# Optimization experiments

Measured on AMD Instinct MI355X. Metric: run time of the kernel, lower is better.

Reference implementation:

```python
import jax, jax.numpy as jnp
import numpy as np

NINP, NHID, NOUT, DT = 128, 768, 128, 1.0
T, B = 256, 256


def setup_inputs() -> dict:
    key = jax.random.key(0)
    ks = jax.random.split(key, 9)
    std = 1.0 / np.sqrt(NHID)
    u = lambda k, shape: jax.random.uniform(k, shape, jnp.float32, -std, std)
    return {
        "input": jax.random.normal(ks[0], (T, B, NINP), jnp.float32),
        "W_inp": u(ks[1], (4 * NHID, NINP)),
        "b_inp": u(ks[2], (4 * NHID,)),
        "W_hid": u(ks[3], (3 * NHID, NHID)),
        "b_hid": u(ks[4], (3 * NHID,)),
        "W_z": u(ks[5], (NHID, NHID)),
        "b_z": u(ks[6], (NHID,)),
        "W_cls": jax.random.normal(ks[7], (NOUT, NHID), jnp.float32) * np.sqrt(2.0 / NHID),
        "b_cls": u(ks[8], (NOUT,)),
    }


def reference(input, W_inp, b_inp, W_hid, b_hid, W_z, b_z, W_cls, b_cls):
    # Precompute input projections for all timesteps: [T, B, 4*NHID]
    inp_proj = jnp.einsum('tbi,hi->tbh', input, W_inp) + b_inp

    def step(carry, xi):
        y, z = carry
        hid = y @ W_hid.T + b_hid                     # [B, 3*NHID]
        i_dt1, i_dt2, i_z, i_y = jnp.split(xi, 4, axis=1)
        h_dt1, h_dt2, h_y = jnp.split(hid, 3, axis=1)
        ms_dt_bar = DT * jax.nn.sigmoid(i_dt1 + h_dt1)
        ms_dt = DT * jax.nn.sigmoid(i_dt2 + h_dt2)
        z = (1.0 - ms_dt) * z + ms_dt * jnp.tanh(i_y + h_y)
        y = (1.0 - ms_dt_bar) * y + ms_dt_bar * jnp.tanh(z @ W_z.T + b_z + i_z)
        return (y, z), None

    y0 = jnp.zeros((input.shape[1], NHID), input.dtype)
    z0 = jnp.zeros_like(y0)
    (y, z), _ = jax.lax.scan(step, (y0, z0), inp_proj)
    return y @ W_cls.T + b_cls
```

## Files before the change

### kernel.cpp

```cpp
#include <hip/hip_runtime.h>
#include <stdint.h>


#define NINP 128
#define NHID 768
#define NOUT 128
#define T_STEPS 256
#define BATCH 256

#define NGRP 8
#define CBLK 24
#define NBLK 192
#define NTHR 256

#define NHTILES 144
#define SBUF 196608
#define WZ_ELEMS (1152 * 512)
#define WI_ELEMS (768 * 512)

typedef short bf16x8 __attribute__((ext_vector_type(8)));
typedef float f32x4 __attribute__((ext_vector_type(4)));

__device__ __forceinline__ unsigned short f2b(float f) {
  union { float f; unsigned u; } x; x.f = f;
  return (unsigned short)((x.u + 0x7fffu + ((x.u >> 16) & 1u)) >> 16);
}
__device__ __forceinline__ float b2f(unsigned short h) {
  union { unsigned u; float f; } x; x.u = ((unsigned)h) << 16; return x.f;
}
__device__ __forceinline__ float fsig(float x) { return 1.0f / (1.0f + __expf(-x)); }
__device__ __forceinline__ float ftanh(float x) {
  float e = __expf(2.0f * x);
  return 1.0f - 2.0f / (e + 1.0f);
}

#define MFMA16(a, b, c) __builtin_amdgcn_mfma_f32_16x16x32_bf16(a, b, c, 0, 0, 0)

#define AL32(p) __hip_atomic_load((const unsigned*)(p), __ATOMIC_RELAXED, __HIP_MEMORY_SCOPE_AGENT)
#define AS32(p, v) __hip_atomic_store((unsigned*)(p), (v), __ATOMIC_RELAXED, __HIP_MEMORY_SCOPE_AGENT)

__device__ __forceinline__ void uld16(bf16x8* dst, const unsigned short* addr) {
  asm volatile("global_load_dwordx4 %0, %1, off sc0 sc1" : "=v"(*dst) : "v"(addr));
}
__device__ __forceinline__ void cld16(bf16x8* dst, const unsigned short* addr) {
  asm volatile("global_load_dwordx4 %0, %1, off" : "=v"(*dst) : "v"(addr));
}
__device__ __forceinline__ void ust16(unsigned short* addr, bf16x8 v) {
  asm volatile("global_store_dwordx4 %0, %1, off sc0 sc1" :: "v"(addr), "v"(v) : "memory");
}
#define WAITV(N) do { \
  asm volatile("s_waitcnt vmcnt(" #N ")" ::: "memory"); \
  __builtin_amdgcn_sched_barrier(0); } while (0)

__device__ __forceinline__ void split8(const float* p, bf16x8* hi, bf16x8* lo) {
  union { bf16x8 v; unsigned short s[8]; } H, L;
#pragma unroll
  for (int e = 0; e < 8; ++e) {
    float v = p[e];
    unsigned short h = f2b(v);
    H.s[e] = h;
    L.s[e] = f2b(v - b2f(h));
  }
  *hi = H.v; *lo = L.v;
}

__global__ __launch_bounds__(256) void conv_w(
    const float* __restrict__ W_z, const float* __restrict__ W_inp,
    unsigned short* __restrict__ Wz, unsigned short* __restrict__ Wi) {
  int idx = blockIdx.x * 256 + threadIdx.x;
  int t = idx >> 9, r = idx & 511;
  int ll = r >> 3, e = r & 7;
  int col16 = ll & 15;
  int kk = ((ll >> 4) * 8) + e;
  if (t < 1152) {
    int kt = t % 24, ct = (t / 24) & 1, c = t / 48;
    Wz[idx] = f2b(W_z[(size_t)(c * 32 + ct * 16 + col16) * NHID + kt * 32 + kk]);
  } else {
    int u = t - 1152;
    int xkt = u & 3, ct = (u >> 2) & 1, seg = (u >> 3) & 3, c = u >> 5;
    Wi[(size_t)u * 512 + r] =
        f2b(W_inp[(size_t)(seg * NHID + c * 32 + ct * 16 + col16) * NINP + xkt * 32 + kk]);
  }
}

__global__ __launch_bounds__(256) void xprep(
    const float* __restrict__ x, unsigned short* __restrict__ XF) {
  int gid = blockIdx.x * 256 + threadIdx.x;
  int lane = gid & 63;
  int rtx = (gid >> 6) & 15;
  int xkt = (gid >> 10) & 3;
  int t = gid >> 12;
  int kg = lane >> 4, r16 = lane & 15;
  int row = rtx * 16 + r16;
  bf16x8 hi, lo;
  split8(x + ((size_t)t * BATCH + row) * NINP + xkt * 32 + kg * 8, &hi, &lo);
  size_t lo_off = (size_t)kg * 128 + r16 * 8;
  *(bf16x8*)(XF + ((((size_t)t * 2 + 0) * 4 + xkt) * 16 + rtx) * 512 + lo_off) = hi;
  *(bf16x8*)(XF + ((((size_t)t * 2 + 1) * 4 + xkt) * 16 + rtx) * 512 + lo_off) = lo;
}

__global__ __launch_bounds__(NTHR, 1) void lem_kernel(
    const float* __restrict__ b_inp,
    const float* __restrict__ W_hid,
    const float* __restrict__ b_hid,
    const float* __restrict__ b_z,
    const float* __restrict__ W_cls,
    const float* __restrict__ b_cls,
    float* __restrict__ out,
    unsigned short* __restrict__ Y,
    unsigned short* __restrict__ Z,
    unsigned* __restrict__ flags,
    const unsigned short* __restrict__ Wz,
    const unsigned short* __restrict__ Wi,
    const unsigned short* __restrict__ XF)
{
  __shared__ unsigned short wlds[NHTILES * 512];
  __shared__ float red[128 * 24];
  __shared__ unsigned short zt[2 * 512];

  const int tid = threadIdx.x;
  const int l   = tid & 63;
  const int w   = tid >> 6;
  const int rtl = w & 1;
  const int kh  = w >> 1;
  const int g   = blockIdx.x / CBLK;
  const int c   = blockIdx.x % CBLK;
  const int colbase = c * 32;
  const int lc  = l & 15;
  const int kg8 = (l >> 4) * 8;
  const int laneoff = (l >> 4) * 128 + lc * 8;
  const int rtg = g * 2 + rtl;
  const int r16b = (l >> 4) * 4;

  for (int idx = tid; idx < NHTILES * 512; idx += NTHR) {
    int t = idx >> 9;
    int r = idx & 511;
    int ll = r >> 3, e = r & 7;
    int col16 = ll & 15;
    int kk = ((ll >> 4) * 8) + e;
    int kt = t % 24, cs = t / 24;
    int ct = cs / 3, seg = cs % 3;
    wlds[idx] = f2b(W_hid[(size_t)(seg * NHID + colbase + ct * 16 + col16) * NHID + kt * 32 + kk]);
  }

#define LDSB(t) (*(const bf16x8*)&wlds[((t) << 9) + (l << 3)])

  float c1[2], c2[2], cy[2], cz[2];
#pragma unroll
  for (int ct = 0; ct < 2; ++ct) {
    int col = colbase + ct * 16 + lc;
    c1[ct] = b_inp[col] + b_hid[col];
    c2[ct] = b_inp[NHID + col] + b_hid[NHID + col];
    cy[ct] = b_inp[3 * NHID + col] + b_hid[2 * NHID + col];
    cz[ct] = b_inp[2 * NHID + col] + b_z[col];
  }
  unsigned* gfA = flags + g * 128;
  unsigned* gfB = gfA + 64;
  const int khb = kh * 12;
  unsigned short* Zc = Z + (size_t)(c * 16 + rtg) * 512;
  unsigned short* Yc = Y + (size_t)(c * 16 + rtg) * 512;

  bf16x8 wifA[3][2][2];
  bf16x8 wiB[2][2];
#pragma unroll
  for (int hseg = 0; hseg < 3; ++hseg) {
    int wseg = (hseg == 2) ? 3 : hseg;
#pragma unroll
    for (int ct = 0; ct < 2; ++ct)
#pragma unroll
      for (int xk2 = 0; xk2 < 2; ++xk2)
        cld16(&wifA[hseg][ct][xk2],
              Wi + (size_t)((((c * 4 + wseg) * 2 + ct) * 4) + (kh * 2 + xk2)) * 512 + l * 8);
  }
#pragma unroll
  for (int ct = 0; ct < 2; ++ct)
#pragma unroll
    for (int xk2 = 0; xk2 < 2; ++xk2)
      cld16(&wiB[ct][xk2],
            Wi + (size_t)((((c * 4 + 2) * 2 + ct) * 4) + (kh * 2 + xk2)) * 512 + l * 8);

  bf16x8 xa[4];
#define ISSUE_XA(sidx) do { \
    cld16(&xa[0], XF + ((((size_t)(sidx) * 2 + 0) * 4 + (kh * 2 + 0)) * 16 + rtg) * 512 + laneoff); \
    cld16(&xa[1], XF + ((((size_t)(sidx) * 2 + 1) * 4 + (kh * 2 + 0)) * 16 + rtg) * 512 + laneoff); \
    cld16(&xa[2], XF + ((((size_t)(sidx) * 2 + 0) * 4 + (kh * 2 + 1)) * 16 + rtg) * 512 + laneoff); \
    cld16(&xa[3], XF + ((((size_t)(sidx) * 2 + 1) * 4 + (kh * 2 + 1)) * 16 + rtg) * 512 + laneoff); } while (0)

  ISSUE_XA(0);
  WAITV(0);
  __syncthreads();

  f32x4 yloc[2], zloc[2], msb[2];
#pragma unroll
  for (int ct = 0; ct < 2; ++ct) { yloc[ct] = f32x4{0,0,0,0}; zloc[ct] = f32x4{0,0,0,0}; }

  float* rp = red + (rtl * 64 + l) * 24;
  unsigned short* trow = zt + rtl * 512;

  bf16x8 ybufs[6][2];
  bf16x8 zbuf[6];
  bf16x8 wzf[6][2];
  const unsigned short* wzb0 = Wz + (size_t)((c * 2 + 0) * 24) * 512 + l * 8;
  const unsigned short* wzb1 = Wz + (size_t)((c * 2 + 1) * 24) * 512 + l * 8;

#define ISSUE_Y(slot, j) do { \
    int kt_ = khb + 2 * (j); \
    uld16(&ybufs[slot][0], Y + (size_t)(kt_ * 16 + rtg) * 512 + laneoff); \
    uld16(&ybufs[slot][1], Y + (size_t)((kt_ + 1) * 16 + rtg) * 512 + laneoff); } while (0)

#define ISSUE_Z(slot, j) do { \
    int kt_ = khb + (j); \
    uld16(&zbuf[slot], Z + (size_t)(kt_ * 16 + rtg) * 512 + laneoff); \
    cld16(&wzf[slot][0], wzb0 + (size_t)kt_ * 512); \
    cld16(&wzf[slot][1], wzb1 + (size_t)kt_ * 512); } while (0)

  for (int s = 0; s < T_STEPS; ++s) {
    f32x4 h[3][2];
#pragma unroll
    for (int sg = 0; sg < 3; ++sg)
#pragma unroll
      for (int ct = 0; ct < 2; ++ct) h[sg][ct] = f32x4{0,0,0,0};

    ISSUE_Y(0, 0); ISSUE_Y(1, 1); ISSUE_Y(2, 2);
    ISSUE_Y(3, 3); ISSUE_Y(4, 4); ISSUE_Y(5, 5);
    WAITV(12);
#pragma unroll
    for (int xk2 = 0; xk2 < 2; ++xk2)
#pragma unroll
      for (int sg = 0; sg < 3; ++sg)
#pragma unroll
        for (int ct = 0; ct < 2; ++ct) {
          h[sg][ct] = MFMA16(xa[xk2 * 2 + 0], wifA[sg][ct][xk2], h[sg][ct]);
          h[sg][ct] = MFMA16(xa[xk2 * 2 + 1], wifA[sg][ct][xk2], h[sg][ct]);
        }
#pragma unroll
    for (int j = 0; j < 6; ++j) {
      if (j == 0) { WAITV(10); } else if (j == 1) { WAITV(8); }
      else if (j == 2) { WAITV(6); } else if (j == 3) { WAITV(4); }
      else if (j == 4) { WAITV(2); } else { WAITV(0); }
#pragma unroll
      for (int i2 = 0; i2 < 2; ++i2) {
        int ktp = khb + 2 * j + i2;
        bf16x8 a = ybufs[j][i2];
#pragma unroll
        for (int ct = 0; ct < 2; ++ct)
#pragma unroll
          for (int sg = 0; sg < 3; ++sg)
            h[sg][ct] = MFMA16(a, LDSB((ct * 3 + sg) * 24 + ktp), h[sg][ct]);
      }
    }
    if (kh == 1) {
#pragma unroll
      for (int sg = 0; sg < 3; ++sg)
#pragma unroll
        for (int ct = 0; ct < 2; ++ct)
          *(f32x4*)(rp + (sg * 2 + ct) * 4) = h[sg][ct];
    }
    __syncthreads();
    if (kh == 0) {
#pragma unroll
      for (int sg = 0; sg < 3; ++sg)
#pragma unroll
        for (int ct = 0; ct < 2; ++ct)
          h[sg][ct] += *(const f32x4*)(rp + (sg * 2 + ct) * 4);
#pragma unroll
      for (int ct = 0; ct < 2; ++ct)
#pragma unroll
        for (int i = 0; i < 4; ++i) {
          float a1 = fsig(h[0][ct][i] + c1[ct]);
          float a2 = fsig(h[1][ct][i] + c2[ct]);
          float gg = ftanh(h[2][ct][i] + cy[ct]);
          float zn = (1.0f - a2) * zloc[ct][i] + a2 * gg;
          zloc[ct][i] = zn;
          msb[ct][i] = a1;
          int jj = ct * 16 + lc;
          trow[((jj >> 3) * 16 + r16b + i) * 8 + (jj & 7)] = f2b(zn);
        }
      asm volatile("s_waitcnt lgkmcnt(0)" ::: "memory");
      __builtin_amdgcn_sched_barrier(0);
      bf16x8 zrun = *(const bf16x8*)(trow + l * 8);
      ust16(Zc + l * 8, zrun);
    }
    __syncthreads();
    if (tid == 0) AS32(&gfA[c], (unsigned)(s + 1));
    if (w == 0) {
      const unsigned* fp = gfA + (l < CBLK ? l : 0);
      while (true) {
        unsigned v = AL32(fp);
        if (__all((l >= CBLK) || (v >= (unsigned)(s + 1)))) break;
        __builtin_amdgcn_s_sleep(1);
      }
    }
    __syncthreads();

    f32x4 az[2];
    az[0] = f32x4{0,0,0,0}; az[1] = f32x4{0,0,0,0};
    ISSUE_Z(0, 0); ISSUE_Z(1, 1); ISSUE_Z(2, 2); ISSUE_Z(3, 3); ISSUE_Z(4, 4);
#pragma unroll
    for (int xk2 = 0; xk2 < 2; ++xk2)
#pragma unroll
      for (int ct = 0; ct < 2; ++ct) {
        az[ct] = MFMA16(xa[xk2 * 2 + 0], wiB[ct][xk2], az[ct]);
        az[ct] = MFMA16(xa[xk2 * 2 + 1], wiB[ct][xk2], az[ct]);
      }
#pragma unroll
    for (int j = 0; j < 12; ++j) {
      if (j < 7) ISSUE_Z((j + 5) % 6, j + 5);
      if (j < 7) { WAITV(15); } else if (j == 7) { WAITV(12); }
      else if (j == 8) { WAITV(9); } else if (j == 9) { WAITV(6); }
      else if (j == 10) { WAITV(3); } else { WAITV(0); }
      const int sl = j % 6;
      az[0] = MFMA16(zbuf[sl], wzf[sl][0], az[0]);
      az[1] = MFMA16(zbuf[sl], wzf[sl][1], az[1]);
    }
    if (kh == 1) {
      *(f32x4*)(rp + 0) = az[0];
      *(f32x4*)(rp + 4) = az[1];
    }
    __syncthreads();
    if (kh == 0) {
      az[0] += *(const f32x4*)(rp + 0);
      az[1] += *(const f32x4*)(rp + 4);
#pragma unroll
      for (int ct = 0; ct < 2; ++ct)
#pragma unroll
        for (int i = 0; i < 4; ++i) {
          float tt = ftanh(az[ct][i] + cz[ct]);
          float yn = (1.0f - msb[ct][i]) * yloc[ct][i] + msb[ct][i] * tt;
          yloc[ct][i] = yn;
          int jj = ct * 16 + lc;
          trow[((jj >> 3) * 16 + r16b + i) * 8 + (jj & 7)] = f2b(yn);
        }
      asm volatile("s_waitcnt lgkmcnt(0)" ::: "memory");
      __builtin_amdgcn_sched_barrier(0);
      bf16x8 yrun = *(const bf16x8*)(trow + l * 8);
      ust16(Yc + l * 8, yrun);
    }
    __syncthreads();
    if (tid == 0) AS32(&gfB[c], (unsigned)(s + 1));
    if (s + 1 < T_STEPS) ISSUE_XA(s + 1);
    if (w == 0) {
      const unsigned* fp = gfB + (l < CBLK ? l : 0);
      while (true) {
        unsigned v = AL32(fp);
        if (__all((l >= CBLK) || (v >= (unsigned)(s + 1)))) break;
        __builtin_amdgcn_s_sleep(1);
      }
    }
    __syncthreads();
  }

  if (c < 8) {
    const int ocb = c * 16;
    f32x4 ao{0, 0, 0, 0};
    bf16x8 yb[12];
#pragma unroll
    for (int j = 0; j < 12; ++j)
      uld16(&yb[j], Y + (size_t)((khb + j) * 16 + rtg) * 512 + laneoff);
    WAITV(0);
#pragma unroll
    for (int j = 0; j < 12; ++j) {
      int kt = khb + j;
      bf16x8 bh, bl;
      split8(W_cls + (size_t)(ocb + lc) * NHID + kt * 32 + kg8, &bh, &bl);
      ao = MFMA16(yb[j], bh, ao);
      ao = MFMA16(yb[j], bl, ao);
    }
    if (kh == 1) *(f32x4*)(rp + 0) = ao;
    __syncthreads();
    if (kh == 0) {
      ao += *(const f32x4*)(rp + 0);
      float bc = b_cls[ocb + lc];
#pragma unroll
      for (int i = 0; i < 4; ++i)
        out[(size_t)(g * 32 + rtl * 16 + r16b + i) * NOUT + ocb + lc] = ao[i] + bc;
    }
  }
}

extern "C" void kernel_launch(void* const* d_in, const int* in_sizes, int n_in,
                              void* d_out, int out_size, void* d_ws, size_t ws_size,
                              hipStream_t stream) {
  (void)in_sizes; (void)n_in; (void)out_size; (void)ws_size;
  const float* x     = (const float*)d_in[0];
  const float* W_inp = (const float*)d_in[1];
  const float* b_inp = (const float*)d_in[2];
  const float* W_hid = (const float*)d_in[3];
  const float* b_hid = (const float*)d_in[4];
  const float* W_z   = (const float*)d_in[5];
  const float* b_z   = (const float*)d_in[6];
  const float* W_cls = (const float*)d_in[7];
  const float* b_cls = (const float*)d_in[8];

  unsigned short* Y = (unsigned short*)d_ws;
  unsigned short* Z = Y + SBUF;
  unsigned* flags = (unsigned*)(Z + SBUF);
  unsigned short* Wz = (unsigned short*)(flags + NGRP * 128);
  unsigned short* Wi = Wz + WZ_ELEMS;
  unsigned short* XF = Wi + WI_ELEMS;

  hipMemsetAsync(d_ws, 0, 2 * SBUF * sizeof(unsigned short) + NGRP * 128 * sizeof(unsigned), stream);

  conv_w<<<dim3(3840), dim3(256), 0, stream>>>(W_z, W_inp, Wz, Wi);
  xprep<<<dim3(4096), dim3(256), 0, stream>>>(x, XF);

  lem_kernel<<<dim3(NBLK), dim3(NTHR), 0, stream>>>(
      b_inp, W_hid, b_hid, b_z, W_cls, b_cls,
      (float*)d_out, Y, Z, flags, Wz, Wi, XF);
}
```

Measured before the change: 2.066 ms.

## Replace block-wide barriers with per-wave flags and all-wave polling

Each producing wave (kh==0, one per row tile) now waits for its own global stores, then publishes its own per-step flag. Every wave polls all 48 flags of the group directly, replacing the two __syncthreads plus single-wave poll around each inter-block exchange. This removes two block barriers per phase per timestep on the serial recurrence critical path. In exchange the flag array doubles in size and every wave spins on global atomics, which adds memory traffic. Correctness relies on the remaining intra-block LDS reuse staying safe without those barriers.

After: 3.301 ms. +59.8%, slower.

```diff
diff --git a/kernel.cpp b/kernel.cpp
--- a/kernel.cpp
+++ b/kernel.cpp
@@ -12,6 +12,7 @@
 #define CBLK 24
 #define NBLK 192
 #define NTHR 256
+#define NFLG (CBLK * 2)
 
 #define NHTILES 144
 #define SBUF 196608
@@ -154,8 +155,8 @@
     cy[ct] = b_inp[3 * NHID + col] + b_hid[2 * NHID + col];
     cz[ct] = b_inp[2 * NHID + col] + b_z[col];
   }
-  unsigned* gfA = flags + g * 128;
-  unsigned* gfB = gfA + 64;
+  unsigned* gfA = flags + g * 256;
+  unsigned* gfB = gfA + 128;
   const int khb = kh * 12;
   unsigned short* Zc = Z + (size_t)(c * 16 + rtg) * 512;
   unsigned short* Yc = Y + (size_t)(c * 16 + rtg) * 512;
@@ -213,6 +214,14 @@
     uld16(&zbuf[slot], Z + (size_t)(kt_ * 16 + rtg) * 512 + laneoff); \
     cld16(&wzf[slot][0], wzb0 + (size_t)kt_ * 512); \
     cld16(&wzf[slot][1], wzb1 + (size_t)kt_ * 512); } while (0)
+
+#define POLL(gf, tgt) do { \
+    const unsigned* fp_ = (gf) + (l < NFLG ? l : 0); \
+    while (true) { \
+      unsigned v_ = AL32(fp_); \
+      if (__all((l >= NFLG) || (v_ >= (unsigned)(tgt)))) break; \
+      __builtin_amdgcn_s_sleep(1); \
+    } } while (0)
 
   for (int s = 0; s < T_STEPS; ++s) {
     f32x4 h[3][2];
@@ -280,18 +289,10 @@
       __builtin_amdgcn_sched_barrier(0);
       bf16x8 zrun = *(const bf16x8*)(trow + l * 8);
       ust16(Zc + l * 8, zrun);
-    }
-    __syncthreads();
-    if (tid == 0) AS32(&gfA[c], (unsigned)(s + 1));
-    if (w == 0) {
-      const unsigned* fp = gfA + (l < CBLK ? l : 0);
-      while (true) {
-        unsigned v = AL32(fp);
-        if (__all((l >= CBLK) || (v >= (unsigned)(s + 1)))) break;
-        __builtin_amdgcn_s_sleep(1);
-      }
-    }
-    __syncthreads();
+      WAITV(0);
+      if (l == 0) AS32(&gfA[c * 2 + rtl], (unsigned)(s + 1));
+    }
+    POLL(gfA, s + 1);
 
     f32x4 az[2];
     az[0] = f32x4{0,0,0,0}; az[1] = f32x4{0,0,0,0};
@@ -335,19 +336,11 @@
       __builtin_amdgcn_sched_barrier(0);
       bf16x8 yrun = *(const bf16x8*)(trow + l * 8);
       ust16(Yc + l * 8, yrun);
-    }
-    __syncthreads();
-    if (tid == 0) AS32(&gfB[c], (unsigned)(s + 1));
+      WAITV(0);
+      if (l == 0) AS32(&gfB[c * 2 + rtl], (unsigned)(s + 1));
+    }
     if (s + 1 < T_STEPS) ISSUE_XA(s + 1);
-    if (w == 0) {
-      const unsigned* fp = gfB + (l < CBLK ? l : 0);
-      while (true) {
-        unsigned v = AL32(fp);
-        if (__all((l >= CBLK) || (v >= (unsigned)(s + 1)))) break;
-        __builtin_amdgcn_s_sleep(1);
-      }
-    }
-    __syncthreads();
+    POLL(gfB, s + 1);
   }
 
   if (c < 8) {
@@ -395,11 +388,11 @@
   unsigned short* Y = (unsigned short*)d_ws;
   unsigned short* Z = Y + SBUF;
   unsigned* flags = (unsigned*)(Z + SBUF);
-  unsigned short* Wz = (unsigned short*)(flags + NGRP * 128);
+  unsigned short* Wz = (unsigned short*)(flags + NGRP * 256);
   unsigned short* Wi = Wz + WZ_ELEMS;
   unsigned short* XF = Wi + WI_ELEMS;
 
-  hipMemsetAsync(d_ws, 0, 2 * SBUF * sizeof(unsigned short) + NGRP * 128 * sizeof(unsigned), stream);
+  hipMemsetAsync(d_ws, 0, 2 * SBUF * sizeof(unsigned short) + NGRP * 256 * sizeof(unsigned), stream);
 
   conv_w<<<dim3(3840), dim3(256), 0, stream>>>(W_z, W_inp, Wz, Wi);
   xprep<<<dim3(4096), dim3(256), 0, stream>>>(x, XF);
```
